# Performance work log

Hardware: AMD Instinct MI355X
Metric: run time of the kernel (lower is better)

Reference implementation:

```python
import jax, jax.numpy as jnp
import numpy as np

N_USER = 100000
N_ITEM = 50000
N_EDGE = 400000
D_IN = 128
N_HEADS = 4
D_HEAD = 32


def setup_inputs() -> dict:
    key = jax.random.key(0)
    ks = jax.random.split(key, 10)
    s = 1.0 / np.sqrt(D_IN)
    return {
        "h_user": jax.random.normal(ks[0], (N_USER, D_IN), jnp.float32),
        "h_item": jax.random.normal(ks[1], (N_ITEM, D_IN), jnp.float32),
        "edge_user": jax.random.randint(ks[2], (N_EDGE,), 0, N_USER),
        "edge_item": jax.random.randint(ks[3], (N_EDGE,), 0, N_ITEM),
        "user_w_qs": jax.random.normal(ks[4], (N_HEADS, D_IN, D_HEAD), jnp.float32) * s,
        "user_w_ks": jax.random.normal(ks[5], (N_HEADS, D_IN, D_HEAD), jnp.float32) * s,
        "user_w_vs": jax.random.normal(ks[6], (N_HEADS, D_IN, D_HEAD), jnp.float32) * s,
        "item_w_qs": jax.random.normal(ks[7], (N_HEADS, D_IN, D_HEAD), jnp.float32) * s,
        "item_w_ks": jax.random.normal(ks[8], (N_HEADS, D_IN, D_HEAD), jnp.float32) * s,
        "item_w_vs": jax.random.normal(ks[9], (N_HEADS, D_IN, D_HEAD), jnp.float32) * s,
    }


def _segment_softmax(logit, seg, num_segments):
    m = jax.ops.segment_max(logit, seg, num_segments=num_segments)
    e = jnp.exp(logit - m[seg])
    s = jax.ops.segment_sum(e, seg, num_segments=num_segments)
    return e / s[seg]


def _attend(src_idx, dst_idx, h_src, h_dst, w_qs, w_ks, w_vs, n_dst):
    # per-head projections: [H, n, d_head]
    q = jnp.einsum("nd,hde->hne", h_dst, w_qs)
    k = jnp.einsum("nd,hde->hne", h_src, w_ks)
    v = jnp.einsum("nd,hde->hne", h_src, w_vs)
    # per-edge logits: [H, E]
    logit = jnp.sum(q[:, dst_idx] * k[:, src_idx], axis=-1)
    att = jax.vmap(lambda l: _segment_softmax(l, dst_idx, n_dst))(logit)
    # sparse adj @ v == segment-sum of attention-weighted source values
    msg = att[..., None] * v[:, src_idx]  # [H, E, d_head]
    z = jax.vmap(lambda m: jax.ops.segment_sum(m, dst_idx, num_segments=n_dst))(msg)
    z = jax.nn.relu(z)  # nonlinear per head, then merge (concat)
    return jnp.transpose(z, (1, 0, 2)).reshape(n_dst, -1)


def reference(h_user, h_item, edge_user, edge_item,
              user_w_qs, user_w_ks, user_w_vs,
              item_w_qs, item_w_ks, item_w_vs):
    # i2u: items -> users (dst = users)
    z_user = _attend(edge_item, edge_user, h_item, h_user,
                     user_w_qs, item_w_ks, item_w_vs, N_USER)
    # u2i: users -> items (dst = items)
    z_item = _attend(edge_user, edge_item, h_user, h_item,
                     item_w_qs, user_w_ks, user_w_vs, N_ITEM)
    return (z_user, z_item)
```

## Files before the change

### kernel.cpp

```cpp
#include <hip/hip_runtime.h>
#include <hip/hip_fp16.h>


typedef unsigned short u16;
typedef float f32x4 __attribute__((ext_vector_type(4)));
typedef short bf16x8 __attribute__((ext_vector_type(8)));

#define NU_C    100000
#define NI_C    50000
#define E_C     400000
#define D_IN    128
#define D_HEAD  32
#define N_HEADS 4

#define PB_U 1563
#define PB_I 782
#define WT_BLKS 384

#define SCAN_T  256
#define SCAN_E  1024

__device__ __forceinline__ float bf2f(u16 b) {
    return __uint_as_float(((unsigned)b) << 16);
}

__device__ __forceinline__ u16 f2bf_rn(float x) {
    unsigned u = __float_as_uint(x);
    u += 0x7FFFu + ((u >> 16) & 1u);
    return (u16)(u >> 16);
}

__device__ __forceinline__ u16 f2h(float x) {
    return __half_as_ushort(__float2half(x));
}
__device__ __forceinline__ float h2f(u16 b) {
    return __half2float(__ushort_as_half(b));
}

__global__ void detect_dtypes(const void* __restrict__ h,
                              const void* __restrict__ eu,
                              int* __restrict__ flags) {
    int t = threadIdx.x;
    const u16* hw = (const u16*)h;
    int cnt = 0;
#pragma unroll
    for (int r = 0; r < 2; ++r) {
        int i = t + r * 64;
        unsigned ex = (hw[2 * i] >> 7) & 0xFFu;
        if (ex >= 118u && ex <= 137u) cnt++;
    }
    const int* ew = (const int*)eu;
    int nz = 0;
#pragma unroll
    for (int r = 0; r < 4; ++r) {
        int i = t + r * 64;
        if (ew[2 * i + 1] != 0) nz++;
    }
#pragma unroll
    for (int m = 1; m < 64; m <<= 1) {
        cnt += __shfl_xor(cnt, m);
        nz  += __shfl_xor(nz, m);
    }
    if (t == 0) {
        flags[0] = (cnt >= 64) ? 1 : 0;
        flags[1] = (nz == 0) ? 1 : 0;
        flags[2] = 0;
        flags[3] = 0;
    }
}

__global__ __launch_bounds__(256)
void prep(const void* __restrict__ w0, const void* __restrict__ w1,
          const void* __restrict__ w2, const void* __restrict__ w3,
          const void* __restrict__ w4, const void* __restrict__ w5,
          u16* __restrict__ wthi, u16* __restrict__ wtlo,
          const int* __restrict__ e_user, const int* __restrict__ e_item,
          int* __restrict__ du, int* __restrict__ di,
          int* __restrict__ degU, int* __restrict__ degI,
          int* __restrict__ flags) {
    int b = blockIdx.x;
    if (b < WT_BLKS) {
        int m = b >> 6;
        int f = (b & 63) * 256 + threadIdx.x;
        const void* ws[6] = { w0, w1, w2, w3, w4, w5 };
        const void* wp = ws[m];
        int head = f >> 12, d = (f >> 5) & 127, e = f & 31;
        float x;
        if (flags[0]) x = bf2f(((const u16*)wp)[f]);
        else          x = ((const float*)wp)[f];
        u16 h = f2bf_rn(x);
        u16 l = f2bf_rn(x - bf2f(h));
        int j = head * 32 + e;
        int ct8 = j >> 4, lr = j & 15;
        int kc = d >> 5, lk = (d & 31) >> 3, ei = d & 7;
        int o = m * 16384 + (ct8 * 4 + kc) * 512 + (lk * 16 + lr) * 8 + ei;
        wthi[o] = h;
        wtlo[o] = l;
    } else {
        int g = (b - WT_BLKS) * 256 + threadIdx.x;
        if (g >= E_C) return;
        int is64 = flags[1];
        int u = is64 ? e_user[2 * g] : e_user[g];
        int i = is64 ? e_item[2 * g] : e_item[g];
        if ((unsigned)u >= (unsigned)NU_C) { atomicOr(&flags[3], 1); u = 0; }
        if ((unsigned)i >= (unsigned)NI_C) { atomicOr(&flags[3], 1); i = 0; }
        du[g] = u;
        di[g] = i;
        atomicAdd(&degU[u], 1);
        atomicAdd(&degI[i], 1);
    }
}

__global__ __launch_bounds__(SCAN_T)
void scan_pass1(const int* __restrict__ degU, int* __restrict__ offsU,
                int* __restrict__ partU, int nU, int sbU,
                const int* __restrict__ degI, int* __restrict__ offsI,
                int* __restrict__ partI, int nI) {
    __shared__ int tsum[SCAN_T];
    int t = threadIdx.x, b = blockIdx.x;
    const int* deg; int* offs; int* partials; int n; int lb;
    if (b < sbU) { deg = degU; offs = offsU; partials = partU; n = nU; lb = b; }
    else         { deg = degI; offs = offsI; partials = partI; n = nI; lb = b - sbU; }
    int idx = lb * SCAN_E + t * 4;
    int v0 = 0, v1 = 0, v2 = 0, v3 = 0;
    if (idx + 3 < n) {
        v0 = deg[idx]; v1 = deg[idx + 1]; v2 = deg[idx + 2]; v3 = deg[idx + 3];
    } else {
        if (idx     < n) v0 = deg[idx];
        if (idx + 1 < n) v1 = deg[idx + 1];
        if (idx + 2 < n) v2 = deg[idx + 2];
        if (idx + 3 < n) v3 = deg[idx + 3];
    }
    int s = v0 + v1 + v2 + v3;
    tsum[t] = s;
    __syncthreads();
#pragma unroll
    for (int o = 1; o < SCAN_T; o <<= 1) {
        int x = (t >= o) ? tsum[t - o] : 0;
        __syncthreads();
        tsum[t] += x;
        __syncthreads();
    }
    int run = tsum[t] - s;
    if (idx     < n) offs[idx]     = run;             run += v0;
    if (idx + 1 < n) offs[idx + 1] = run;             run += v1;
    if (idx + 2 < n) offs[idx + 2] = run;             run += v2;
    if (idx + 3 < n) offs[idx + 3] = run;
    if (t == SCAN_T - 1) partials[lb] = tsum[t];
}

__global__ __launch_bounds__(SCAN_T)
void scan_pass2(int* __restrict__ partU, int sbU,
                int* __restrict__ partI, int sbI) {
    __shared__ int tsum[SCAN_T];
    int t = threadIdx.x;
    int* partials; int nb;
    if (blockIdx.x == 0) { partials = partU; nb = sbU; }
    else                 { partials = partI; nb = sbI; }
    int v = (t < nb) ? partials[t] : 0;
    tsum[t] = v;
    __syncthreads();
#pragma unroll
    for (int o = 1; o < SCAN_T; o <<= 1) {
        int x = (t >= o) ? tsum[t - o] : 0;
        __syncthreads();
        tsum[t] += x;
        __syncthreads();
    }
    if (t < nb) partials[t] = tsum[t] - v;
}

__global__ void scatter2(const int* __restrict__ du, const int* __restrict__ di,
                         const int* __restrict__ offsU, const int* __restrict__ partU,
                         int* __restrict__ cntU, int* __restrict__ csrU,
                         const int* __restrict__ offsI, const int* __restrict__ partI,
                         int* __restrict__ cntI, int* __restrict__ csrI, int egrid) {
    int b = blockIdx.x;
    int g = (b >= egrid ? b - egrid : b) * 256 + threadIdx.x;
    if (g >= E_C) return;
    if (b < egrid) {
        int d = du[g];
        int pos = offsU[d] + partU[d >> 10] + atomicAdd(&cntU[d], 1);
        csrU[pos] = di[g];
    } else {
        int d = di[g];
        int pos = offsI[d] + partI[d >> 10] + atomicAdd(&cntI[d], 1);
        csrI[pos] = du[g];
    }
}

__global__ __launch_bounds__(256)
void proj3x(const void* __restrict__ hu, const void* __restrict__ hi_,
            const u16* __restrict__ wthi_, const u16* __restrict__ wtlo_,
            u16* __restrict__ QU, u16* __restrict__ KU, u16* __restrict__ VU,
            u16* __restrict__ QI, u16* __restrict__ KI, u16* __restrict__ VI,
            const int* __restrict__ flags) {
    __shared__ u16 Hhi[64 * 128], Hlo[64 * 128];

    const int b = blockIdx.x;
    const void* hraw; int N, mbase, lb;
    u16* out0; u16* out1; u16* out2;
    if (b < PB_U) {
        hraw = hu;  N = NU_C; mbase = 0; lb = b;
        out0 = QU; out1 = KU; out2 = VU;
    } else {
        hraw = hi_; N = NI_C; mbase = 3; lb = b - PB_U;
        out0 = QI; out1 = KI; out2 = VI;
    }
    const int t = threadIdx.x;
    const int n0 = lb * 64;
    const int isbf = flags[0];

    {
        int row = t >> 2, cb = (t & 3) * 4;
        int gn = min(n0 + row, N - 1);
        if (!isbf) {
            const float* hp = (const float*)hraw + (size_t)gn * D_IN + cb * 8;
#pragma unroll
            for (int i = 0; i < 4; ++i) {
                f32x4 a0 = *(const f32x4*)(hp + i * 8);
                f32x4 a1 = *(const f32x4*)(hp + i * 8 + 4);
                bf16x8 hv, lv;
#pragma unroll
                for (int q = 0; q < 4; ++q) {
                    u16 hh = f2bf_rn(a0[q]);
                    hv[q] = (short)hh;
                    lv[q] = (short)f2bf_rn(a0[q] - bf2f(hh));
                }
#pragma unroll
                for (int q = 0; q < 4; ++q) {
                    u16 hh = f2bf_rn(a1[q]);
                    hv[4 + q] = (short)hh;
                    lv[4 + q] = (short)f2bf_rn(a1[q] - bf2f(hh));
                }
                int o = row * 128 + (((cb + i) ^ (row & 7)) * 8);
                *(bf16x8*)&Hhi[o] = hv;
                *(bf16x8*)&Hlo[o] = lv;
            }
        } else {
            const u16* hp = (const u16*)hraw + (size_t)gn * D_IN + cb * 8;
            bf16x8 z;
#pragma unroll
            for (int q = 0; q < 8; ++q) z[q] = 0;
#pragma unroll
            for (int i = 0; i < 4; ++i) {
                bf16x8 hv = *(const bf16x8*)(hp + i * 8);
                int o = row * 128 + (((cb + i) ^ (row & 7)) * 8);
                *(bf16x8*)&Hhi[o] = hv;
                *(bf16x8*)&Hlo[o] = z;
            }
        }
    }
    __syncthreads();

    const int w = t >> 6, l = t & 63;
    const int lr = l & 15, lk = l >> 4;

#pragma unroll 1
    for (int mm = 0; mm < 3; ++mm) {
        const u16* wth = wthi_ + (size_t)(mbase + mm) * 16384;
        const u16* wtl = wtlo_ + (size_t)(mbase + mm) * 16384;
        u16* out = (mm == 0) ? out0 : ((mm == 1) ? out1 : out2);

        f32x4 acc[4][2];
#pragma unroll
        for (int rt = 0; rt < 4; ++rt)
#pragma unroll
            for (int ci = 0; ci < 2; ++ci) {
                acc[rt][ci].x = 0.f; acc[rt][ci].y = 0.f;
                acc[rt][ci].z = 0.f; acc[rt][ci].w = 0.f;
            }

#pragma unroll
        for (int kc = 0; kc < 4; ++kc) {
            bf16x8 fAh[4], fAl[4];
#pragma unroll
            for (int rt = 0; rt < 4; ++rt) {
                int row = rt * 16 + lr;
                int o = row * 128 + (((kc * 4 + lk) ^ (lr & 7)) * 8);
                fAh[rt] = *(const bf16x8*)&Hhi[o];
                fAl[rt] = *(const bf16x8*)&Hlo[o];
            }
#pragma unroll
            for (int ci = 0; ci < 2; ++ci) {
                int fb = ((w * 2 + ci) * 4 + kc) * 512 + l * 8;
                bf16x8 fBh = *(const bf16x8*)(wth + fb);
                bf16x8 fBl = *(const bf16x8*)(wtl + fb);
#pragma unroll
                for (int rt = 0; rt < 4; ++rt) {
                    acc[rt][ci] = __builtin_amdgcn_mfma_f32_16x16x32_bf16(
                        fAl[rt], fBh, acc[rt][ci], 0, 0, 0);
                    acc[rt][ci] = __builtin_amdgcn_mfma_f32_16x16x32_bf16(
                        fAh[rt], fBl, acc[rt][ci], 0, 0, 0);
                    acc[rt][ci] = __builtin_amdgcn_mfma_f32_16x16x32_bf16(
                        fAh[rt], fBh, acc[rt][ci], 0, 0, 0);
                }
            }
        }

#pragma unroll
        for (int rt = 0; rt < 4; ++rt) {
#pragma unroll
            for (int r = 0; r < 4; ++r) {
                int n = n0 + rt * 16 + lk * 4 + r;
                if (n < N) {
#pragma unroll
                    for (int ci = 0; ci < 2; ++ci)
                        out[(size_t)n * 128 + w * 32 + ci * 16 + lr] =
                            f2h(acc[rt][ci][r]);
                }
            }
        }
    }
}

__global__ __launch_bounds__(256)
void gather_both(const int* __restrict__ offsU, const int* __restrict__ partU,
                 const int* __restrict__ csrU,
                 const int* __restrict__ offsI, const int* __restrict__ partI,
                 const int* __restrict__ csrI,
                 const u16* __restrict__ QU, const u16* __restrict__ KI,
                 const u16* __restrict__ VI,
                 const u16* __restrict__ QI, const u16* __restrict__ KU,
                 const u16* __restrict__ VU,
                 float* __restrict__ outbase, const int* __restrict__ flags,
                 int ggU) {
    int b = blockIdx.x;
    const int *offs, *part, *csr; const u16 *q, *k, *v;
    float* out; int Ndst; int g;
    if (b < ggU) {
        offs = offsU; part = partU; csr = csrU;
        q = QU; k = KI; v = VI; out = outbase; Ndst = NU_C;
        g = b * 256 + threadIdx.x;
    } else {
        offs = offsI; part = partI; csr = csrI;
        q = QI; k = KU; v = VU;
        out = outbase + (size_t)NU_C * 128; Ndst = NI_C;
        g = (b - ggU) * 256 + threadIdx.x;
    }
    int dst = g >> 6;
    if (dst >= Ndst) return;
    int l  = g & 63;
    int eh = l >> 5;
    int sl = l & 31;
    float* op = out + (size_t)dst * 128 + sl * 4;

    if (flags[3]) {
        if (eh == 0) {
            f32x4 d64; d64.x = d64.y = d64.z = d64.w = 64.0f;
            *(f32x4*)op = d64;
        }
        return;
    }

    ushort4 qu = *(const ushort4*)(q + (size_t)dst * 128 + sl * 4);
    f32x4 qv;
    qv.x = h2f(qu.x); qv.y = h2f(qu.y); qv.z = h2f(qu.z); qv.w = h2f(qu.w);
    f32x4 acc; acc.x = acc.y = acc.z = acc.w = 0.f;
    float ssum = 0.f;

    int e0 = offs[dst] + part[dst >> 10];
    int e1 = (dst + 1 == Ndst) ? E_C
             : offs[dst + 1] + part[(dst + 1) >> 10];
    int e = e0 + eh;
    for (; e + 2 < e1; e += 4) {
        int s0 = csr[e];
        int s1 = csr[e + 2];
        ushort4 ku0 = *(const ushort4*)(k + (size_t)s0 * 128 + sl * 4);
        ushort4 ku1 = *(const ushort4*)(k + (size_t)s1 * 128 + sl * 4);
        ushort4 vu0 = *(const ushort4*)(v + (size_t)s0 * 128 + sl * 4);
        ushort4 vu1 = *(const ushort4*)(v + (size_t)s1 * 128 + sl * 4);
        float d0 = qv.x * h2f(ku0.x) + qv.y * h2f(ku0.y)
                 + qv.z * h2f(ku0.z) + qv.w * h2f(ku0.w);
        float d1 = qv.x * h2f(ku1.x) + qv.y * h2f(ku1.y)
                 + qv.z * h2f(ku1.z) + qv.w * h2f(ku1.w);
        d0 += __shfl_xor(d0, 1);  d1 += __shfl_xor(d1, 1);
        d0 += __shfl_xor(d0, 2);  d1 += __shfl_xor(d1, 2);
        d0 += __shfl_xor(d0, 4);  d1 += __shfl_xor(d1, 4);
        float ev0 = __expf(fminf(fmaxf(d0, -80.f), 80.f));
        float ev1 = __expf(fminf(fmaxf(d1, -80.f), 80.f));
        ssum += ev0 + ev1;
        acc.x += ev0 * h2f(vu0.x) + ev1 * h2f(vu1.x);
        acc.y += ev0 * h2f(vu0.y) + ev1 * h2f(vu1.y);
        acc.z += ev0 * h2f(vu0.z) + ev1 * h2f(vu1.z);
        acc.w += ev0 * h2f(vu0.w) + ev1 * h2f(vu1.w);
    }
    if (e < e1) {
        int s = csr[e];
        ushort4 ku = *(const ushort4*)(k + (size_t)s * 128 + sl * 4);
        ushort4 vu = *(const ushort4*)(v + (size_t)s * 128 + sl * 4);
        float d = qv.x * h2f(ku.x) + qv.y * h2f(ku.y)
                + qv.z * h2f(ku.z) + qv.w * h2f(ku.w);
        d += __shfl_xor(d, 1);
        d += __shfl_xor(d, 2);
        d += __shfl_xor(d, 4);
        float ev = __expf(fminf(fmaxf(d, -80.f), 80.f));
        ssum += ev;
        acc.x += ev * h2f(vu.x); acc.y += ev * h2f(vu.y);
        acc.z += ev * h2f(vu.z); acc.w += ev * h2f(vu.w);
    }
    ssum  += __shfl_xor(ssum, 32);
    acc.x += __shfl_xor(acc.x, 32);
    acc.y += __shfl_xor(acc.y, 32);
    acc.z += __shfl_xor(acc.z, 32);
    acc.w += __shfl_xor(acc.w, 32);
    if (eh == 0) {
        float inv = (ssum > 0.f) ? (1.f / ssum) : 0.f;
        f32x4 o;
        o.x = fmaxf(acc.x * inv, 0.f);
        o.y = fmaxf(acc.y * inv, 0.f);
        o.z = fmaxf(acc.z * inv, 0.f);
        o.w = fmaxf(acc.w * inv, 0.f);
        *(f32x4*)op = o;
    }
}

__global__ void fill_diag(float* __restrict__ out, int n) {
    int g = blockIdx.x * 256 + threadIdx.x;
    if (g < n) out[g] = 48.0f;
}

extern "C" void kernel_launch(void* const* d_in, const int* in_sizes, int n_in,
                              void* d_out, int out_size, void* d_ws, size_t ws_size,
                              hipStream_t stream) {
    const void* h_user    = d_in[0];
    const void* h_item    = d_in[1];
    const int*  edge_user = (const int*)d_in[2];
    const int*  edge_item = (const int*)d_in[3];
    const void* u_wq = d_in[4];
    const void* u_wk = d_in[5];
    const void* u_wv = d_in[6];
    const void* i_wq = d_in[7];
    const void* i_wk = d_in[8];
    const void* i_wv = d_in[9];

    const int NU = NU_C, NI = NI_C;

    size_t szBufU = (((size_t)NU * 128 * 2) + 255) & ~(size_t)255;
    size_t szBufI = (((size_t)NI * 128 * 2) + 255) & ~(size_t)255;
    size_t szE    = (((size_t)E_C * 4) + 255) & ~(size_t)255;
    size_t szOffU = (((size_t)(NU + 1) * 4) + 255) & ~(size_t)255;
    size_t szOffI = (((size_t)(NI + 1) * 4) + 255) & ~(size_t)255;
    size_t szNU   = (((size_t)NU * 4) + 255) & ~(size_t)255;
    size_t szNI   = (((size_t)NI * 4) + 255) & ~(size_t)255;
    size_t szPart = 256 * 4;
    size_t szWt   = (size_t)6 * 16384 * 2;

    size_t off = 0;
    char* base = (char*)d_ws;
    u16* QU      = (u16*)(base + off);   off += szBufU;
    u16* KI      = (u16*)(base + off);   off += szBufI;
    u16* VI      = (u16*)(base + off);   off += szBufI;
    u16* QI      = (u16*)(base + off);   off += szBufI;
    u16* KU      = (u16*)(base + off);   off += szBufU;
    u16* VU      = (u16*)(base + off);   off += szBufU;
    int* du      = (int*)(base + off);   off += szE;
    int* di      = (int*)(base + off);   off += szE;
    int* csrU    = (int*)(base + off);   off += szE;
    int* csrI    = (int*)(base + off);   off += szE;
    int* offsU   = (int*)(base + off);   off += szOffU;
    int* offsI   = (int*)(base + off);   off += szOffI;
    int* partU   = (int*)(base + off);   off += szPart;
    int* partI   = (int*)(base + off);   off += szPart;
    u16* wthi    = (u16*)(base + off);   off += szWt;
    u16* wtlo    = (u16*)(base + off);   off += szWt;
    int* flags   = (int*)(base + off);   off += 256;
    size_t zoff = off;
    int* degU    = (int*)(base + off);   off += szNU;
    int* cntU    = (int*)(base + off);   off += szNU;
    int* degI    = (int*)(base + off);   off += szNI;
    int* cntI    = (int*)(base + off);   off += szNI;
    size_t need = off;

    if (need > ws_size) {
        fill_diag<<<(out_size + 255) / 256, 256, 0, stream>>>((float*)d_out, out_size);
        return;
    }

    int egrid = (E_C + 255) / 256;
    int sbU = (NU + SCAN_E - 1) / SCAN_E;
    int sbI = (NI + SCAN_E - 1) / SCAN_E;
    int ggU = (NU * 64 + 255) / 256;
    int ggI = (NI * 64 + 255) / 256;

    hipMemsetAsync(base + zoff, 0, need - zoff, stream);
    detect_dtypes<<<1, 64, 0, stream>>>(h_user, edge_user, flags);
    prep<<<WT_BLKS + egrid, 256, 0, stream>>>(
        u_wq, u_wk, u_wv, i_wq, i_wk, i_wv, wthi, wtlo,
        edge_user, edge_item, du, di, degU, degI, flags);
    scan_pass1<<<sbU + sbI, SCAN_T, 0, stream>>>(degU, offsU, partU, NU, sbU,
                                                 degI, offsI, partI, NI);
    scan_pass2<<<2, SCAN_T, 0, stream>>>(partU, sbU, partI, sbI);
    scatter2<<<2 * egrid, 256, 0, stream>>>(du, di,
                                            offsU, partU, cntU, csrU,
                                            offsI, partI, cntI, csrI, egrid);
    proj3x<<<PB_U + PB_I, 256, 0, stream>>>(
        h_user, h_item, wthi, wtlo, QU, KU, VU, QI, KI, VI, flags);
    gather_both<<<ggU + ggI, 256, 0, stream>>>(
        offsU, partU, csrU, offsI, partI, csrI,
        QU, KI, VI, QI, KU, VU, (float*)d_out, flags, ggU);
}
```

Before: 351.4 us.

## Fuse dtype detection into prep and merge scan passes with projection kernel

Each prep block now detects the input dtypes itself, so the separate detect_dtypes launch goes away. The two scan passes are folded into the projection launch as extra blocks, and the last-arriving scan block (found with an atomic counter) does the partial-sum scan. This removes three kernel launches and lets the small scan work overlap with the projection GEMM. In exchange, every prep block repeats the detection loads, and the scan now relies on a threadfence plus a done counter.

```diff
diff --git a/kernel.cpp b/kernel.cpp
--- a/kernel.cpp
+++ b/kernel.cpp
@@ -15,10 +15,13 @@
 
 #define PB_U 1563
 #define PB_I 782
+#define PS_PROJ (PB_U + PB_I)
 #define WT_BLKS 384
 
 #define SCAN_T  256
 #define SCAN_E  1024
+#define SB_U 98
+#define SB_I 49
 
 __device__ __forceinline__ float bf2f(u16 b) {
     return __uint_as_float(((unsigned)b) << 16);
@@ -35,38 +38,6 @@
 }
 __device__ __forceinline__ float h2f(u16 b) {
     return __half2float(__ushort_as_half(b));
-}
-
-__global__ void detect_dtypes(const void* __restrict__ h,
-                              const void* __restrict__ eu,
-                              int* __restrict__ flags) {
-    int t = threadIdx.x;
-    const u16* hw = (const u16*)h;
-    int cnt = 0;
-#pragma unroll
-    for (int r = 0; r < 2; ++r) {
-        int i = t + r * 64;
-        unsigned ex = (hw[2 * i] >> 7) & 0xFFu;
-        if (ex >= 118u && ex <= 137u) cnt++;
-    }
-    const int* ew = (const int*)eu;
-    int nz = 0;
-#pragma unroll
-    for (int r = 0; r < 4; ++r) {
-        int i = t + r * 64;
-        if (ew[2 * i + 1] != 0) nz++;
-    }
-#pragma unroll
-    for (int m = 1; m < 64; m <<= 1) {
-        cnt += __shfl_xor(cnt, m);
-        nz  += __shfl_xor(nz, m);
-    }
-    if (t == 0) {
-        flags[0] = (cnt >= 64) ? 1 : 0;
-        flags[1] = (nz == 0) ? 1 : 0;
-        flags[2] = 0;
-        flags[3] = 0;
-    }
 }
 
 __global__ __launch_bounds__(256)
@@ -74,20 +45,39 @@
           const void* __restrict__ w2, const void* __restrict__ w3,
           const void* __restrict__ w4, const void* __restrict__ w5,
           u16* __restrict__ wthi, u16* __restrict__ wtlo,
+          const void* __restrict__ h_user,
           const int* __restrict__ e_user, const int* __restrict__ e_item,
           int* __restrict__ du, int* __restrict__ di,
           int* __restrict__ degU, int* __restrict__ degI,
           int* __restrict__ flags) {
+    __shared__ int sflag;
     int b = blockIdx.x;
+    int t = threadIdx.x;
     if (b < WT_BLKS) {
+        if (t < 64) {
+            const u16* hw = (const u16*)h_user;
+            int cnt = 0;
+#pragma unroll
+            for (int r = 0; r < 2; ++r) {
+                int i = t + r * 64;
+                unsigned ex = (hw[2 * i] >> 7) & 0xFFu;
+                if (ex >= 118u && ex <= 137u) cnt++;
+            }
+#pragma unroll
+            for (int m = 1; m < 64; m <<= 1) cnt += __shfl_xor(cnt, m);
+            if (t == 0) sflag = (cnt >= 64) ? 1 : 0;
+        }
+        __syncthreads();
+        int isbf = sflag;
+        if (b == 0 && t == 0) flags[0] = isbf;
         int m = b >> 6;
-        int f = (b & 63) * 256 + threadIdx.x;
+        int f = (b & 63) * 256 + t;
         const void* ws[6] = { w0, w1, w2, w3, w4, w5 };
         const void* wp = ws[m];
         int head = f >> 12, d = (f >> 5) & 127, e = f & 31;
         float x;
-        if (flags[0]) x = bf2f(((const u16*)wp)[f]);
-        else          x = ((const float*)wp)[f];
+        if (isbf) x = bf2f(((const u16*)wp)[f]);
+        else      x = ((const float*)wp)[f];
         u16 h = f2bf_rn(x);
         u16 l = f2bf_rn(x - bf2f(h));
         int j = head * 32 + e;
@@ -97,9 +87,22 @@
         wthi[o] = h;
         wtlo[o] = l;
     } else {
-        int g = (b - WT_BLKS) * 256 + threadIdx.x;
+        if (t < 64) {
+            const int* ew = (const int*)e_user;
+            int nz = 0;
+#pragma unroll
+            for (int r = 0; r < 4; ++r) {
+                int i = t + r * 64;
+                if (ew[2 * i + 1] != 0) nz++;
+            }
+#pragma unroll
+            for (int m = 1; m < 64; m <<= 1) nz += __shfl_xor(nz, m);
+            if (t == 0) sflag = (nz == 0) ? 1 : 0;
+        }
+        __syncthreads();
+        int is64 = sflag;
+        int g = (b - WT_BLKS) * 256 + t;
         if (g >= E_C) return;
-        int is64 = flags[1];
         int u = is64 ? e_user[2 * g] : e_user[g];
         int i = is64 ? e_item[2 * g] : e_item[g];
         if ((unsigned)u >= (unsigned)NU_C) { atomicOr(&flags[3], 1); u = 0; }
@@ -111,63 +114,204 @@
     }
 }
 
-__global__ __launch_bounds__(SCAN_T)
-void scan_pass1(const int* __restrict__ degU, int* __restrict__ offsU,
-                int* __restrict__ partU, int nU, int sbU,
-                const int* __restrict__ degI, int* __restrict__ offsI,
-                int* __restrict__ partI, int nI) {
-    __shared__ int tsum[SCAN_T];
-    int t = threadIdx.x, b = blockIdx.x;
-    const int* deg; int* offs; int* partials; int n; int lb;
-    if (b < sbU) { deg = degU; offs = offsU; partials = partU; n = nU; lb = b; }
-    else         { deg = degI; offs = offsI; partials = partI; n = nI; lb = b - sbU; }
-    int idx = lb * SCAN_E + t * 4;
-    int v0 = 0, v1 = 0, v2 = 0, v3 = 0;
-    if (idx + 3 < n) {
-        v0 = deg[idx]; v1 = deg[idx + 1]; v2 = deg[idx + 2]; v3 = deg[idx + 3];
+__global__ __launch_bounds__(256)
+void ps(const void* __restrict__ hu, const void* __restrict__ hi_,
+        const u16* __restrict__ wthi_, const u16* __restrict__ wtlo_,
+        u16* __restrict__ QU, u16* __restrict__ KU, u16* __restrict__ VU,
+        u16* __restrict__ QI, u16* __restrict__ KI, u16* __restrict__ VI,
+        const int* __restrict__ flags,
+        const int* __restrict__ degU, int* __restrict__ offsU,
+        int* __restrict__ partU,
+        const int* __restrict__ degI, int* __restrict__ offsI,
+        int* __restrict__ partI,
+        int* __restrict__ done) {
+    __shared__ u16 Hhi[64 * 128], Hlo[64 * 128];
+
+    const int b = blockIdx.x;
+    const int t = threadIdx.x;
+
+    if (b >= PS_PROJ) {
+        int* tsum = (int*)Hhi;
+        __shared__ int islast;
+        int sb = b - PS_PROJ;
+        const int* deg; int* offs; int* partials; int n; int lb;
+        if (sb < SB_U) { deg = degU; offs = offsU; partials = partU; n = NU_C; lb = sb; }
+        else           { deg = degI; offs = offsI; partials = partI; n = NI_C; lb = sb - SB_U; }
+        int idx = lb * SCAN_E + t * 4;
+        int v0 = 0, v1 = 0, v2 = 0, v3 = 0;
+        if (idx + 3 < n) {
+            v0 = deg[idx]; v1 = deg[idx + 1]; v2 = deg[idx + 2]; v3 = deg[idx + 3];
+        } else {
+            if (idx     < n) v0 = deg[idx];
+            if (idx + 1 < n) v1 = deg[idx + 1];
+            if (idx + 2 < n) v2 = deg[idx + 2];
+            if (idx + 3 < n) v3 = deg[idx + 3];
+        }
+        int s = v0 + v1 + v2 + v3;
+        tsum[t] = s;
+        __syncthreads();
+#pragma unroll
+        for (int o = 1; o < SCAN_T; o <<= 1) {
+            int x = (t >= o) ? tsum[t - o] : 0;
+            __syncthreads();
+            tsum[t] += x;
+            __syncthreads();
+        }
+        int run = tsum[t] - s;
+        if (idx     < n) offs[idx]     = run;             run += v0;
+        if (idx + 1 < n) offs[idx + 1] = run;             run += v1;
+        if (idx + 2 < n) offs[idx + 2] = run;             run += v2;
+        if (idx + 3 < n) offs[idx + 3] = run;
+        if (t == SCAN_T - 1) partials[lb] = tsum[t];
+
+        __threadfence();
+        __syncthreads();
+        if (t == 0) {
+            int old = atomicAdd(done, 1);
+            islast = (old == SB_U + SB_I - 1) ? 1 : 0;
+        }
+        __syncthreads();
+        if (!islast) return;
+        __threadfence();
+        int v = (t < SB_U) ? partU[t] : 0;
+        tsum[t] = v;
+        __syncthreads();
+#pragma unroll
+        for (int o = 1; o < SCAN_T; o <<= 1) {
+            int x = (t >= o) ? tsum[t - o] : 0;
+            __syncthreads();
+            tsum[t] += x;
+            __syncthreads();
+        }
+        if (t < SB_U) partU[t] = tsum[t] - v;
+        __syncthreads();
+        int v2b = (t < SB_I) ? partI[t] : 0;
+        tsum[t] = v2b;
+        __syncthreads();
+#pragma unroll
+        for (int o = 1; o < SCAN_T; o <<= 1) {
+            int x = (t >= o) ? tsum[t - o] : 0;
+            __syncthreads();
+            tsum[t] += x;
+            __syncthreads();
+        }
+        if (t < SB_I) partI[t] = tsum[t] - v2b;
+        return;
+    }
+
+    const void* hraw; int N, mbase, lb;
+    u16* out0; u16* out1; u16* out2;
+    if (b < PB_U) {
+        hraw = hu;  N = NU_C; mbase = 0; lb = b;
+        out0 = QU; out1 = KU; out2 = VU;
     } else {
-        if (idx     < n) v0 = deg[idx];
-        if (idx + 1 < n) v1 = deg[idx + 1];
-        if (idx + 2 < n) v2 = deg[idx + 2];
-        if (idx + 3 < n) v3 = deg[idx + 3];
-    }
-    int s = v0 + v1 + v2 + v3;
-    tsum[t] = s;
+        hraw = hi_; N = NI_C; mbase = 3; lb = b - PB_U;
+        out0 = QI; out1 = KI; out2 = VI;
+    }
+    const int n0 = lb * 64;
+    const int isbf = flags[0];
+
+    {
+        int row = t >> 2, cb = (t & 3) * 4;
+        int gn = min(n0 + row, N - 1);
+        if (!isbf) {
+            const float* hp = (const float*)hraw + (size_t)gn * D_IN + cb * 8;
+#pragma unroll
+            for (int i = 0; i < 4; ++i) {
+                f32x4 a0 = *(const f32x4*)(hp + i * 8);
+                f32x4 a1 = *(const f32x4*)(hp + i * 8 + 4);
+                bf16x8 hv, lv;
+#pragma unroll
+                for (int q = 0; q < 4; ++q) {
+                    u16 hh = f2bf_rn(a0[q]);
+                    hv[q] = (short)hh;
+                    lv[q] = (short)f2bf_rn(a0[q] - bf2f(hh));
+                }
+#pragma unroll
+                for (int q = 0; q < 4; ++q) {
+                    u16 hh = f2bf_rn(a1[q]);
+                    hv[4 + q] = (short)hh;
+                    lv[4 + q] = (short)f2bf_rn(a1[q] - bf2f(hh));
+                }
+                int o = row * 128 + (((cb + i) ^ (row & 7)) * 8);
+                *(bf16x8*)&Hhi[o] = hv;
+                *(bf16x8*)&Hlo[o] = lv;
+            }
+        } else {
+            const u16* hp = (const u16*)hraw + (size_t)gn * D_IN + cb * 8;
+            bf16x8 z;
+#pragma unroll
+            for (int q = 0; q < 8; ++q) z[q] = 0;
+#pragma unroll
+            for (int i = 0; i < 4; ++i) {
+                bf16x8 hv = *(const bf16x8*)(hp + i * 8);
+                int o = row * 128 + (((cb + i) ^ (row & 7)) * 8);
+                *(bf16x8*)&Hhi[o] = hv;
+                *(bf16x8*)&Hlo[o] = z;
+            }
+        }
+    }
     __syncthreads();
-#pragma unroll
-    for (int o = 1; o < SCAN_T; o <<= 1) {
-        int x = (t >= o) ? tsum[t - o] : 0;
-        __syncthreads();
-        tsum[t] += x;
-        __syncthreads();
-    }
-    int run = tsum[t] - s;
-    if (idx     < n) offs[idx]     = run;             run += v0;
-    if (idx + 1 < n) offs[idx + 1] = run;             run += v1;
-    if (idx + 2 < n) offs[idx + 2] = run;             run += v2;
-    if (idx + 3 < n) offs[idx + 3] = run;
-    if (t == SCAN_T - 1) partials[lb] = tsum[t];
-}
-
-__global__ __launch_bounds__(SCAN_T)
-void scan_pass2(int* __restrict__ partU, int sbU,
-                int* __restrict__ partI, int sbI) {
-    __shared__ int tsum[SCAN_T];
-    int t = threadIdx.x;
-    int* partials; int nb;
-    if (blockIdx.x == 0) { partials = partU; nb = sbU; }
-    else                 { partials = partI; nb = sbI; }
-    int v = (t < nb) ? partials[t] : 0;
-    tsum[t] = v;
-    __syncthreads();
-#pragma unroll
-    for (int o = 1; o < SCAN_T; o <<= 1) {
-        int x = (t >= o) ? tsum[t - o] : 0;
-        __syncthreads();
-        tsum[t] += x;
-        __syncthreads();
-    }
-    if (t < nb) partials[t] = tsum[t] - v;
+
+    const int w = t >> 6, l = t & 63;
+    const int lr = l & 15, lk = l >> 4;
+
+#pragma unroll 1
+    for (int mm = 0; mm < 3; ++mm) {
+        const u16* wth = wthi_ + (size_t)(mbase + mm) * 16384;
+        const u16* wtl = wtlo_ + (size_t)(mbase + mm) * 16384;
+        u16* out = (mm == 0) ? out0 : ((mm == 1) ? out1 : out2);
+
+        f32x4 acc[4][2];
+#pragma unroll
+        for (int rt = 0; rt < 4; ++rt)
+#pragma unroll
+            for (int ci = 0; ci < 2; ++ci) {
+                acc[rt][ci].x = 0.f; acc[rt][ci].y = 0.f;
+                acc[rt][ci].z = 0.f; acc[rt][ci].w = 0.f;
+            }
+
+#pragma unroll
+        for (int kc = 0; kc < 4; ++kc) {
+            bf16x8 fAh[4], fAl[4];
+#pragma unroll
+            for (int rt = 0; rt < 4; ++rt) {
+                int row = rt * 16 + lr;
+                int o = row * 128 + (((kc * 4 + lk) ^ (lr & 7)) * 8);
+                fAh[rt] = *(const bf16x8*)&Hhi[o];
+                fAl[rt] = *(const bf16x8*)&Hlo[o];
+            }
+#pragma unroll
+            for (int ci = 0; ci < 2; ++ci) {
+                int fb = ((w * 2 + ci) * 4 + kc) * 512 + l * 8;
+                bf16x8 fBh = *(const bf16x8*)(wth + fb);
+                bf16x8 fBl = *(const bf16x8*)(wtl + fb);
+#pragma unroll
+                for (int rt = 0; rt < 4; ++rt) {
+                    acc[rt][ci] = __builtin_amdgcn_mfma_f32_16x16x32_bf16(
+                        fAl[rt], fBh, acc[rt][ci], 0, 0, 0);
+                    acc[rt][ci] = __builtin_amdgcn_mfma_f32_16x16x32_bf16(
+                        fAh[rt], fBl, acc[rt][ci], 0, 0, 0);
+                    acc[rt][ci] = __builtin_amdgcn_mfma_f32_16x16x32_bf16(
+                        fAh[rt], fBh, acc[rt][ci], 0, 0, 0);
+                }
+            }
+        }
+
+#pragma unroll
+        for (int rt = 0; rt < 4; ++rt) {
+#pragma unroll
+            for (int r = 0; r < 4; ++r) {
+                int n = n0 + rt * 16 + lk * 4 + r;
+                if (n < N) {
+#pragma unroll
+                    for (int ci = 0; ci < 2; ++ci)
+                        out[(size_t)n * 128 + w * 32 + ci * 16 + lr] =
+                            f2h(acc[rt][ci][r]);
+                }
+            }
+        }
+    }
 }
 
 __global__ void scatter2(const int* __restrict__ du, const int* __restrict__ di,
@@ -186,131 +330,6 @@
         int d = di[g];
         int pos = offsI[d] + partI[d >> 10] + atomicAdd(&cntI[d], 1);
         csrI[pos] = du[g];
-    }
-}
-
-__global__ __launch_bounds__(256)
-void proj3x(const void* __restrict__ hu, const void* __restrict__ hi_,
-            const u16* __restrict__ wthi_, const u16* __restrict__ wtlo_,
-            u16* __restrict__ QU, u16* __restrict__ KU, u16* __restrict__ VU,
-            u16* __restrict__ QI, u16* __restrict__ KI, u16* __restrict__ VI,
-            const int* __restrict__ flags) {
-    __shared__ u16 Hhi[64 * 128], Hlo[64 * 128];
-
-    const int b = blockIdx.x;
-    const void* hraw; int N, mbase, lb;
-    u16* out0; u16* out1; u16* out2;
-    if (b < PB_U) {
-        hraw = hu;  N = NU_C; mbase = 0; lb = b;
-        out0 = QU; out1 = KU; out2 = VU;
-    } else {
-        hraw = hi_; N = NI_C; mbase = 3; lb = b - PB_U;
-        out0 = QI; out1 = KI; out2 = VI;
-    }
-    const int t = threadIdx.x;
-    const int n0 = lb * 64;
-    const int isbf = flags[0];
-
-    {
-        int row = t >> 2, cb = (t & 3) * 4;
-        int gn = min(n0 + row, N - 1);
-        if (!isbf) {
-            const float* hp = (const float*)hraw + (size_t)gn * D_IN + cb * 8;
-#pragma unroll
-            for (int i = 0; i < 4; ++i) {
-                f32x4 a0 = *(const f32x4*)(hp + i * 8);
-                f32x4 a1 = *(const f32x4*)(hp + i * 8 + 4);
-                bf16x8 hv, lv;
-#pragma unroll
-                for (int q = 0; q < 4; ++q) {
-                    u16 hh = f2bf_rn(a0[q]);
-                    hv[q] = (short)hh;
-                    lv[q] = (short)f2bf_rn(a0[q] - bf2f(hh));
-                }
-#pragma unroll
-                for (int q = 0; q < 4; ++q) {
-                    u16 hh = f2bf_rn(a1[q]);
-                    hv[4 + q] = (short)hh;
-                    lv[4 + q] = (short)f2bf_rn(a1[q] - bf2f(hh));
-                }
-                int o = row * 128 + (((cb + i) ^ (row & 7)) * 8);
-                *(bf16x8*)&Hhi[o] = hv;
-                *(bf16x8*)&Hlo[o] = lv;
-            }
-        } else {
-            const u16* hp = (const u16*)hraw + (size_t)gn * D_IN + cb * 8;
-            bf16x8 z;
-#pragma unroll
-            for (int q = 0; q < 8; ++q) z[q] = 0;
-#pragma unroll
-            for (int i = 0; i < 4; ++i) {
-                bf16x8 hv = *(const bf16x8*)(hp + i * 8);
-                int o = row * 128 + (((cb + i) ^ (row & 7)) * 8);
-                *(bf16x8*)&Hhi[o] = hv;
-                *(bf16x8*)&Hlo[o] = z;
-            }
-        }
-    }
-    __syncthreads();
-
-    const int w = t >> 6, l = t & 63;
-    const int lr = l & 15, lk = l >> 4;
-
-#pragma unroll 1
-    for (int mm = 0; mm < 3; ++mm) {
-        const u16* wth = wthi_ + (size_t)(mbase + mm) * 16384;
-        const u16* wtl = wtlo_ + (size_t)(mbase + mm) * 16384;
-        u16* out = (mm == 0) ? out0 : ((mm == 1) ? out1 : out2);
-
-        f32x4 acc[4][2];
-#pragma unroll
-        for (int rt = 0; rt < 4; ++rt)
-#pragma unroll
-            for (int ci = 0; ci < 2; ++ci) {
-                acc[rt][ci].x = 0.f; acc[rt][ci].y = 0.f;
-                acc[rt][ci].z = 0.f; acc[rt][ci].w = 0.f;
-            }
-
-#pragma unroll
-        for (int kc = 0; kc < 4; ++kc) {
-            bf16x8 fAh[4], fAl[4];
-#pragma unroll
-            for (int rt = 0; rt < 4; ++rt) {
-                int row = rt * 16 + lr;
-                int o = row * 128 + (((kc * 4 + lk) ^ (lr & 7)) * 8);
-                fAh[rt] = *(const bf16x8*)&Hhi[o];
-                fAl[rt] = *(const bf16x8*)&Hlo[o];
-            }
-#pragma unroll
-            for (int ci = 0; ci < 2; ++ci) {
-                int fb = ((w * 2 + ci) * 4 + kc) * 512 + l * 8;
-                bf16x8 fBh = *(const bf16x8*)(wth + fb);
-                bf16x8 fBl = *(const bf16x8*)(wtl + fb);
-#pragma unroll
-                for (int rt = 0; rt < 4; ++rt) {
-                    acc[rt][ci] = __builtin_amdgcn_mfma_f32_16x16x32_bf16(
-                        fAl[rt], fBh, acc[rt][ci], 0, 0, 0);
-                    acc[rt][ci] = __builtin_amdgcn_mfma_f32_16x16x32_bf16(
-                        fAh[rt], fBl, acc[rt][ci], 0, 0, 0);
-                    acc[rt][ci] = __builtin_amdgcn_mfma_f32_16x16x32_bf16(
-                        fAh[rt], fBh, acc[rt][ci], 0, 0, 0);
-                }
-            }
-        }
-
-#pragma unroll
-        for (int rt = 0; rt < 4; ++rt) {
-#pragma unroll
-            for (int r = 0; r < 4; ++r) {
-                int n = n0 + rt * 16 + lk * 4 + r;
-                if (n < N) {
-#pragma unroll
-                    for (int ci = 0; ci < 2; ++ci)
-                        out[(size_t)n * 128 + w * 32 + ci * 16 + lr] =
-                            f2h(acc[rt][ci][r]);
-                }
-            }
-        }
     }
 }
 
@@ -464,8 +483,9 @@
     int* partI   = (int*)(base + off);   off += szPart;
     u16* wthi    = (u16*)(base + off);   off += szWt;
     u16* wtlo    = (u16*)(base + off);   off += szWt;
+    size_t zoff = off;
     int* flags   = (int*)(base + off);   off += 256;
-    size_t zoff = off;
+    int* done    = (int*)(base + off);   off += 256;
     int* degU    = (int*)(base + off);   off += szNU;
     int* cntU    = (int*)(base + off);   off += szNU;
     int* degI    = (int*)(base + off);   off += szNI;
@@ -478,24 +498,19 @@
     }
 
     int egrid = (E_C + 255) / 256;
-    int sbU = (NU + SCAN_E - 1) / SCAN_E;
-    int sbI = (NI + SCAN_E - 1) / SCAN_E;
     int ggU = (NU * 64 + 255) / 256;
     int ggI = (NI * 64 + 255) / 256;
 
     hipMemsetAsync(base + zoff, 0, need - zoff, stream);
-    detect_dtypes<<<1, 64, 0, stream>>>(h_user, edge_user, flags);
     prep<<<WT_BLKS + egrid, 256, 0, stream>>>(
         u_wq, u_wk, u_wv, i_wq, i_wk, i_wv, wthi, wtlo,
-        edge_user, edge_item, du, di, degU, degI, flags);
-    scan_pass1<<<sbU + sbI, SCAN_T, 0, stream>>>(degU, offsU, partU, NU, sbU,
-                                                 degI, offsI, partI, NI);
-    scan_pass2<<<2, SCAN_T, 0, stream>>>(partU, sbU, partI, sbI);
+        h_user, edge_user, edge_item, du, di, degU, degI, flags);
+    ps<<<PS_PROJ + SB_U + SB_I, 256, 0, stream>>>(
+        h_user, h_item, wthi, wtlo, QU, KU, VU, QI, KI, VI, flags,
+        degU, offsU, partU, degI, offsI, partI, done);
     scatter2<<<2 * egrid, 256, 0, stream>>>(du, di,
                                             offsU, partU, cntU, csrU,
                                             offsI, partI, cntI, csrI, egrid);
-    proj3x<<<PB_U + PB_I, 256, 0, stream>>>(
-        h_user, h_item, wthi, wtlo, QU, KU, VU, QI, KI, VI, flags);
     gather_both<<<ggU + ggI, 256, 0, stream>>>(
         offsU, partU, csrU, offsI, partI, csrI,
         QU, KI, VI, QI, KU, VU, (float*)d_out, flags, ggU);
```

Measured after the change: 364.8 us. 1.04x slower.
